# Kernel optimization log

Measured on AMD Instinct MI355X. Metric: run time of the kernel, lower is better.

The kernel has to match this reference:

```python
import jax, jax.numpy as jnp
import numpy as np

N, E, C = 100000, 50000, 256
M, D, F, T = 128, 128, 128, 64
MSG = 2 * D + F + T  # 448
T_MAX = 100000


def setup_inputs() -> dict:
    key = jax.random.key(0)
    ks = jax.random.split(key, 16)
    src = jax.random.randint(ks[0], (E,), 0, N, dtype=jnp.int32)
    dst = jax.random.randint(ks[1], (E,), 0, N, dtype=jnp.int32)
    t = jnp.sort(jax.random.randint(ks[2], (E,), 0, T_MAX, dtype=jnp.int32))
    last_update = jax.random.randint(ks[3], (N,), 0, 1000, dtype=jnp.int32)
    event_feat = jax.random.normal(ks[4], (E, F), dtype=jnp.float32)
    src_embeds = jax.random.normal(ks[5], (E, D), dtype=jnp.float32)
    dst_embeds = jax.random.normal(ks[6], (E, D), dtype=jnp.float32)
    nodes_memory = jax.random.normal(ks[7], (N, M), dtype=jnp.float32)
    incidence = jax.random.uniform(ks[8], (N, C), dtype=jnp.float32)
    w_time = jax.random.normal(ks[9], (T,), dtype=jnp.float32)
    b_time = jax.random.normal(ks[10], (T,), dtype=jnp.float32)
    W_ih = jax.random.normal(ks[11], (MSG, 3 * M), dtype=jnp.float32) * 0.05
    W_hh = jax.random.normal(ks[12], (M, 3 * M), dtype=jnp.float32) * 0.05
    b_ih = jnp.zeros((3 * M,), jnp.float32)
    b_hh = jnp.zeros((3 * M,), jnp.float32)
    return dict(src=src, dst=dst, t=t, last_update=last_update,
                event_feat=event_feat, src_embeds=src_embeds, dst_embeds=dst_embeds,
                nodes_memory=nodes_memory, incidence=incidence,
                w_time=w_time, b_time=b_time, W_ih=W_ih, W_hh=W_hh,
                b_ih=b_ih, b_hh=b_hh)


def reference(src, dst, t, last_update, event_feat, src_embeds, dst_embeds,
              nodes_memory, incidence, w_time, b_time, W_ih, W_hh, b_ih, b_hh):
    E2 = 2 * E
    # store_events: raw messages + flipped-direction messages, keyed by source node
    src_all = jnp.concatenate([src, dst])            # [2E]
    emb_s = jnp.concatenate([src_embeds, dst_embeds], axis=0)
    emb_d = jnp.concatenate([dst_embeds, src_embeds], axis=0)
    feat = jnp.concatenate([event_feat, event_feat], axis=0)
    t_all = jnp.concatenate([t, t])                  # [2E]
    # message function: concat(src_embed, dst_embed, event_feat, time_encoding(dt))
    dt = (t_all - last_update[src_all]).astype(jnp.float32)
    time_enc = jnp.cos(dt[:, None] * w_time[None, :] + b_time[None, :])  # [2E, T]
    msg = jnp.concatenate([emb_s, emb_d, feat, time_enc], axis=-1)       # [2E, MSG]
    # 'last' aggregation: per-node argmax over timestamps via rank-encoded segment_max
    perm = jnp.argsort(t_all)  # ascending time order
    rank = jnp.zeros((E2,), jnp.int32).at[perm].set(jnp.arange(E2, dtype=jnp.int32))
    seg_rank = jax.ops.segment_max(rank, src_all, num_segments=N)
    counts = jax.ops.segment_sum(jnp.ones((E2,), jnp.int32), src_all, num_segments=N)
    has_msg = counts > 0                              # [N]
    last_idx = perm[jnp.where(has_msg, seg_rank, 0)]  # [N] event index of last message
    agg_msg = msg[last_idx]                           # [N, MSG]
    # GRU memory updater (torch.nn.GRUCell convention)
    gx = agg_msg @ W_ih + b_ih
    gh = nodes_memory @ W_hh + b_hh
    xr, xz, xn = jnp.split(gx, 3, axis=-1)
    hr, hz, hn = jnp.split(gh, 3, axis=-1)
    r = jax.nn.sigmoid(xr + hr)
    z = jax.nn.sigmoid(xz + hz)
    n = jnp.tanh(xn + r * hn)
    h_new = (1.0 - z) * n + z * nodes_memory
    new_mem = jnp.where(has_msg[:, None], h_new, nodes_memory)  # [N, M]
    # rewire_graph: community memory = incidence.T @ nodes_memory
    comm_mem = jnp.einsum('nc,nm->cm', incidence, new_mem)      # [C, M]
    return jnp.concatenate([new_mem, comm_mem], axis=0)         # [N + C, M]
```

## Files before the change

### kernel.cpp

```cpp
#include <hip/hip_runtime.h>
#include <hip/hip_bf16.h>
#include <stdint.h>

#define N_NODES   100000
#define N_EVENTS  50000
#define N_COMM    256
#define DIM_M     128
#define K_TOT     576
#define GCOLS     512
#define INV2PI    0.15915494309189535f
#define XB_GRID   2048
#define WCONV_BLOCKS ((GCOLS * K_TOT + 255) / 256)
#define COPY_BLOCKS  512

typedef float f32x4 __attribute__((ext_vector_type(4)));
typedef short s16x8 __attribute__((ext_vector_type(8)));
typedef short s16x4 __attribute__((ext_vector_type(4)));

#define KEYS_OFF   0
#define CNT_OFF    800000
#define LIST_OFF   800008
#define EINFO_OFF  1200064
#define WT_OFF     2800128
#define X_ROWS     100096
#define X_OFF      3390208
#define PART_M_OFF X_OFF
#define CT_NCH     512
#define CT_CPN     196
#define TMP2_OFF   (PART_M_OFF + 67108864)
#define WT_F_OFF   1200640
#define TENC_OFF   1790464
#define PART_F_OFF 14594560

__device__ inline unsigned short f2bf(float x) {
    union { float f; unsigned u; } v; v.f = x;
    unsigned r = v.u + 0x7FFFu + ((v.u >> 16) & 1u);
    return (unsigned short)(r >> 16);
}
__device__ inline float bf2f(unsigned short u) {
    union { unsigned u; float f; } v; v.u = ((unsigned)u) << 16;
    return v.f;
}
__device__ inline float cos_rev(float rev) {
    float fr = rev - floorf(rev);
#if __has_builtin(__builtin_amdgcn_cosf)
    return __builtin_amdgcn_cosf(fr);
#else
    return cosf(fr * 6.283185307179586f);
#endif
}
__device__ inline float sigmoid_f(float x) { return 1.0f / (1.0f + __expf(-x)); }
__device__ inline float tanh_f(float x) {
    float t = __expf(2.0f * x);
    return 1.0f - 2.0f / (t + 1.0f);
}
__device__ inline s16x8 pack_bf8(float4 a, float4 b) {
    s16x8 v;
    v[0] = (short)f2bf(a.x); v[1] = (short)f2bf(a.y);
    v[2] = (short)f2bf(a.z); v[3] = (short)f2bf(a.w);
    v[4] = (short)f2bf(b.x); v[5] = (short)f2bf(b.y);
    v[6] = (short)f2bf(b.z); v[7] = (short)f2bf(b.w);
    return v;
}

__global__ __launch_bounds__(256) void k_agg(const int* __restrict__ src,
                                             const int* __restrict__ dst,
                                             const int* __restrict__ t,
                                             unsigned long long* __restrict__ keys) {
    int i = blockIdx.x * 256 + threadIdx.x;
    if (i >= 2 * N_EVENTS) return;
    int e = (i < N_EVENTS) ? i : i - N_EVENTS;
    int node = (i < N_EVENTS) ? src[i] : dst[e];
    unsigned long long key =
        ((unsigned long long)(unsigned)t[e] << 32) | (unsigned)(i + 1);
    atomicMax(&keys[node], key);
}

__global__ __launch_bounds__(256) void k_compact(const unsigned long long* __restrict__ keys,
                                                 const int* __restrict__ t,
                                                 const int* __restrict__ last_update,
                                                 unsigned int* __restrict__ cnt,
                                                 int* __restrict__ list,
                                                 int4* __restrict__ einfo) {
    int n = blockIdx.x * 256 + threadIdx.x;
    if (n >= N_NODES) return;
    const unsigned long long key = keys[n];
    if (key != 0ULL) {
        unsigned p = atomicAdd(cnt, 1u);
        list[p] = n;
        const int ia = (int)(key & 0xffffffffull) - 1;
        const int e = (ia < N_EVENTS) ? ia : ia - N_EVENTS;
        const float dt = (float)(t[e] - last_update[n]);
        einfo[p] = make_int4(n, ia, __float_as_int(dt), 0);
    }
}

__global__ __launch_bounds__(256) void k_xbuild(
    const unsigned long long* __restrict__ keys,
    const unsigned int* __restrict__ cnt,
    const int4* __restrict__ einfo,
    const float* __restrict__ event_feat,
    const float* __restrict__ src_embeds,
    const float* __restrict__ dst_embeds,
    const float* __restrict__ mem,
    const float* __restrict__ w_time,
    const float* __restrict__ b_time,
    const float* __restrict__ W_ih,
    const float* __restrict__ W_hh,
    unsigned short* __restrict__ Wt,
    unsigned short* __restrict__ X,
    float* __restrict__ out) {
    if (blockIdx.x >= XB_GRID + WCONV_BLOCKS) {
        const int b = blockIdx.x - (XB_GRID + WCONV_BLOCKS);
        for (int idx = b * 256 + threadIdx.x; idx < N_NODES * 32;
             idx += COPY_BLOCKS * 256) {
            const int n = idx >> 5;
            if (keys[n] == 0ULL)
                ((float4*)out)[idx] = ((const float4*)mem)[idx];
        }
        return;
    }
    if (blockIdx.x >= XB_GRID) {
        int idx = (blockIdx.x - XB_GRID) * 256 + threadIdx.x;
        if (idx >= GCOLS * K_TOT) return;
        int col2 = idx / K_TOT, k = idx % K_TOT;
        int mh = col2 >> 8, rem = col2 & 255;
        int g = rem >> 6, m = mh * 64 + (rem & 63);
        float v;
        if (g == 0)      v = (k < 448) ? W_ih[(size_t)k * 384 + m]
                                       : W_hh[(size_t)(k - 448) * 384 + m];
        else if (g == 1) v = (k < 448) ? W_ih[(size_t)k * 384 + 128 + m]
                                       : W_hh[(size_t)(k - 448) * 384 + 128 + m];
        else if (g == 2) v = (k < 448) ? W_ih[(size_t)k * 384 + 256 + m] : 0.0f;
        else             v = (k < 448) ? 0.0f : W_hh[(size_t)(k - 448) * 384 + 256 + m];
        Wt[idx] = f2bf(v);
        return;
    }
    const unsigned c = *cnt;
    const unsigned cpad = (c + 127u) & ~127u;
    const int l8 = threadIdx.x & 7;
    const int off = l8 * 8;
    for (unsigned row = (blockIdx.x * 256u + threadIdx.x) >> 3; row < cpad;
         row += (XB_GRID * 256u) >> 3) {
        unsigned short* xp = X + (size_t)row * K_TOT + off;
        if (row >= c) {
            s16x8 z;
#pragma unroll
            for (int q = 0; q < 8; ++q) z[q] = 0;
#pragma unroll
            for (int j = 0; j < 9; ++j) *(s16x8*)(xp + j * 64) = z;
            continue;
        }
        const int4 ei = einfo[row];
        const int ia = ei.y;
        const int e = (ia < N_EVENTS) ? ia : ia - N_EVENTS;
        const float* sp = src_embeds + (size_t)e * 128;
        const float* dp = dst_embeds + (size_t)e * 128;
        const float* pe_s = (ia < N_EVENTS) ? sp : dp;
        const float* pe_d = (ia < N_EVENTS) ? dp : sp;
        const float* pe_f = event_feat + (size_t)e * 128;
        const float* pm   = mem + (size_t)ei.x * 128;
        const float* ps[8] = {pe_s, pe_s + 64, pe_d, pe_d + 64,
                              pe_f, pe_f + 64, pm,   pm + 64};
        float4 d0[8], d1[8];
#pragma unroll
        for (int j = 0; j < 8; ++j) {
            d0[j] = *(const float4*)(ps[j] + off);
            d1[j] = *(const float4*)(ps[j] + off + 4);
        }
        const float dt = __int_as_float(ei.z);
        s16x8 tv;
#pragma unroll
        for (int q = 0; q < 8; ++q) {
            float rev = fmaf(dt, w_time[off + q] * INV2PI, b_time[off + q] * INV2PI);
            tv[q] = (short)f2bf(cos_rev(rev));
        }
#pragma unroll
        for (int j = 0; j < 6; ++j)
            *(s16x8*)(xp + j * 64) = pack_bf8(d0[j], d1[j]);
        *(s16x8*)(xp + 6 * 64) = tv;
        *(s16x8*)(xp + 7 * 64) = pack_bf8(d0[6], d1[6]);
        *(s16x8*)(xp + 8 * 64) = pack_bf8(d0[7], d1[7]);
    }
}

__global__ __launch_bounds__(512, 4) void k_gemm2(
    const unsigned int* __restrict__ cnt,
    const int* __restrict__ list,
    const unsigned short* __restrict__ X,
    const unsigned short* __restrict__ Wt,
    const float* __restrict__ b_ih,
    const float* __restrict__ b_hh,
    float* __restrict__ out) {
    __shared__ unsigned short As[3][128][32];
    __shared__ unsigned short Bs[3][256][32];
    __shared__ int Ls[128];

    const unsigned c = *cnt;
    const int rb = blockIdx.x >> 1;
    const int mh = blockIdx.x & 1;
    const int base = rb * 128;
    if ((unsigned)base >= c) return;
    const int tid = threadIdx.x;
    const int w = tid >> 6, l = tid & 63;
    const int lr = l & 15, lk = l >> 4;
    const int wm = w >> 2, wn = w & 3;

    if (tid < 128)
        Ls[tid] = ((unsigned)(base + tid) < c) ? list[base + tid] : 0;

    const int mcol = mh * 64 + wn * 16 + lr;

    unsigned short hreg[16];
#pragma unroll
    for (int rt = 0; rt < 4; ++rt)
#pragma unroll
        for (int reg = 0; reg < 4; ++reg) {
            const int r = wm * 64 + rt * 16 + lk * 4 + reg;
            hreg[rt * 4 + reg] = X[(size_t)(base + r) * K_TOT + 448 + mcol];
        }

    const int srow = tid >> 2;
    const int sd = tid & 3;
    const int ssl = (sd ^ ((srow >> 1) & 3)) << 3;
    const unsigned short* gA  = X  + (size_t)(base + srow) * K_TOT + ssl;
    const unsigned short* gB0 = Wt + (size_t)(mh * 256 + srow) * K_TOT + ssl;
    const unsigned short* gB1 = Wt + (size_t)(mh * 256 + 128 + srow) * K_TOT + ssl;

#define GLD(SRC, DST) __builtin_amdgcn_global_load_lds( \
        (const __attribute__((address_space(1))) unsigned int*)(SRC), \
        (__attribute__((address_space(3))) unsigned int*)(DST), 16, 0, 0)

    auto stage = [&](int ch, int buf) {
        GLD(gA  + ch * 32, &As[buf][w * 16][0]);
        GLD(gB0 + ch * 32, &Bs[buf][w * 16][0]);
        GLD(gB1 + ch * 32, &Bs[buf][128 + w * 16][0]);
    };

    f32x4 acc[4][4];
#pragma unroll
    for (int rt = 0; rt < 4; ++rt)
#pragma unroll
        for (int i = 0; i < 4; ++i) acc[rt][i] = (f32x4){0.f, 0.f, 0.f, 0.f};

    stage(0, 0);
    stage(1, 1);
    __syncthreads();

#pragma unroll
    for (int ch = 0; ch < 18; ++ch) {
        const int buf = ch % 3;
        if (ch <= 15) stage(ch + 2, (ch + 2) % 3);
        __builtin_amdgcn_s_setprio(1);
        s16x8 a[4];
#pragma unroll
        for (int rt = 0; rt < 4; ++rt) {
            const int r = wm * 64 + rt * 16 + lr;
            const int sl = lk ^ ((r >> 1) & 3);
            a[rt] = *(const s16x8*)&As[buf][r][sl << 3];
        }
#pragma unroll
        for (int i = 0; i < 4; ++i) {
            const int cl = i * 64 + wn * 16 + lr;
            const int slb = lk ^ ((cl >> 1) & 3);
            s16x8 b = *(const s16x8*)&Bs[buf][cl][slb << 3];
#pragma unroll
            for (int rt = 0; rt < 4; ++rt)
                acc[rt][i] = __builtin_amdgcn_mfma_f32_16x16x32_bf16(
                    a[rt], b, acc[rt][i], 0, 0, 0);
        }
        __builtin_amdgcn_s_setprio(0);
        if (ch < 17) {
            __builtin_amdgcn_sched_barrier(0);
            if (ch < 16) asm volatile("s_waitcnt vmcnt(3)" ::: "memory");
            else         asm volatile("s_waitcnt vmcnt(0)" ::: "memory");
            __builtin_amdgcn_s_barrier();
            __builtin_amdgcn_sched_barrier(0);
        }
    }

    const float b_r  = b_ih[mcol] + b_hh[mcol];
    const float b_z  = b_ih[128 + mcol] + b_hh[128 + mcol];
    const float b_xn = b_ih[256 + mcol];
    const float b_hn = b_hh[256 + mcol];
#pragma unroll
    for (int rt = 0; rt < 4; ++rt) {
#pragma unroll
        for (int reg = 0; reg < 4; ++reg) {
            const int r = wm * 64 + rt * 16 + lk * 4 + reg;
            const int grow = base + r;
            if ((unsigned)grow < c) {
                const int node = Ls[r];
                const float h = bf2f(hreg[rt * 4 + reg]);
                float rr = sigmoid_f(acc[rt][0][reg] + b_r);
                float zz = sigmoid_f(acc[rt][1][reg] + b_z);
                float nn = tanh_f(acc[rt][2][reg] + b_xn + rr * (acc[rt][3][reg] + b_hn));
                out[(size_t)node * 128 + mcol] = (1.0f - zz) * nn + zz * h;
            }
        }
    }
#undef GLD
}

__global__ __launch_bounds__(256) void k_copy(const unsigned long long* __restrict__ keys,
                                              const float* __restrict__ nm,
                                              float* __restrict__ out) {
    int idx = blockIdx.x * 256 + threadIdx.x;
    int n = idx >> 5;
    if (n >= N_NODES) return;
    if (keys[n] != 0ULL) return;
    ((float4*)out)[idx] = ((const float4*)nm)[idx];
}

__global__ __launch_bounds__(512) void k_comm_t(const float* __restrict__ inc,
                                                const float* __restrict__ nm,
                                                float* __restrict__ partials) {
    __shared__ unsigned short T[2][12288];

    const int bid = blockIdx.x;
    const int n0 = bid * CT_CPN;
    const int n1 = min(N_NODES, n0 + CT_CPN);
    const int ng = (n1 - n0 + 31) >> 5;
    const int tid = threadIdx.x;
    const int w = tid >> 6, l = tid & 63;
    const int lr = l & 15, lk = l >> 4;

    float vi[4][4];
    float vm[4][2];

    auto load_chunk = [&](int g) {
        const int nb = n0 + g * 32 + w * 4;
#pragma unroll
        for (int ri = 0; ri < 4; ++ri) {
            const int n = nb + ri;
            const bool ok = n < n1;
#pragma unroll
            for (int j = 0; j < 4; ++j)
                vi[ri][j] = ok ? inc[(size_t)n * N_COMM + l + 64 * j] : 0.0f;
#pragma unroll
            for (int j = 0; j < 2; ++j)
                vm[ri][j] = ok ? nm[(size_t)n * DIM_M + l + 64 * j] : 0.0f;
        }
    };
    auto write_chunk = [&](int buf) {
        unsigned short* bi = &T[buf][0];
#pragma unroll
        for (int j = 0; j < 4; ++j) {
            const int cc = l + 64 * j;
            ushort4 p = make_ushort4(f2bf(vi[0][j]), f2bf(vi[1][j]),
                                     f2bf(vi[2][j]), f2bf(vi[3][j]));
            *(ushort4*)&bi[cc * 32 + ((w ^ (cc & 7)) << 2)] = p;
        }
        unsigned short* bm = &T[buf][8192];
#pragma unroll
        for (int j = 0; j < 2; ++j) {
            const int mm = l + 64 * j;
            ushort4 p = make_ushort4(f2bf(vm[0][j]), f2bf(vm[1][j]),
                                     f2bf(vm[2][j]), f2bf(vm[3][j]));
            *(ushort4*)&bm[mm * 32 + ((w ^ (mm & 7)) << 2)] = p;
        }
    };

    f32x4 acc[2][8];
#pragma unroll
    for (int ct = 0; ct < 2; ++ct)
#pragma unroll
        for (int mt = 0; mt < 8; ++mt) acc[ct][mt] = (f32x4){0.f, 0.f, 0.f, 0.f};

    auto compute_chunk = [&](int buf) {
        const unsigned short* bi = &T[buf][0];
        const unsigned short* bm = &T[buf][8192];
        s16x8 a[2];
#pragma unroll
        for (int ct = 0; ct < 2; ++ct) {
            const int cc = (w * 2 + ct) * 16 + lr;
            s16x4 lo = *(const s16x4*)&bi[cc * 32 + (((lk * 2) ^ (cc & 7)) << 2)];
            s16x4 hi = *(const s16x4*)&bi[cc * 32 + (((lk * 2 + 1) ^ (cc & 7)) << 2)];
            a[ct] = __builtin_shufflevector(lo, hi, 0, 1, 2, 3, 4, 5, 6, 7);
        }
#pragma unroll
        for (int mt = 0; mt < 8; ++mt) {
            const int mm = mt * 16 + lr;
            s16x4 lo = *(const s16x4*)&bm[mm * 32 + (((lk * 2) ^ (mm & 7)) << 2)];
            s16x4 hi = *(const s16x4*)&bm[mm * 32 + (((lk * 2 + 1) ^ (mm & 7)) << 2)];
            s16x8 b = __builtin_shufflevector(lo, hi, 0, 1, 2, 3, 4, 5, 6, 7);
            acc[0][mt] = __builtin_amdgcn_mfma_f32_16x16x32_bf16(a[0], b, acc[0][mt], 0, 0, 0);
            acc[1][mt] = __builtin_amdgcn_mfma_f32_16x16x32_bf16(a[1], b, acc[1][mt], 0, 0, 0);
        }
    };

    load_chunk(0);
    write_chunk(0);
    __syncthreads();
    for (int g = 0; g < ng; ++g) {
        if (g + 1 < ng) load_chunk(g + 1);
        compute_chunk(g & 1);
        if (g + 1 < ng) write_chunk((g + 1) & 1);
        __syncthreads();
    }

    float* p = partials + (size_t)bid * (N_COMM * DIM_M);
#pragma unroll
    for (int ct = 0; ct < 2; ++ct)
#pragma unroll
        for (int mt = 0; mt < 8; ++mt)
            *(f32x4*)&p[(size_t)(((ct * 8 + mt) * 512) + tid) * 4] = acc[ct][mt];
}

__global__ __launch_bounds__(256) void k_comm2a(const float* __restrict__ partials,
                                                float* __restrict__ tmp) {
    const int bid = blockIdx.x;
    const int y = bid >> 5, x = bid & 31;
    const int idx4 = x * 256 + threadIdx.x;
    float4 s = make_float4(0.f, 0.f, 0.f, 0.f);
    for (int ci = 0; ci < CT_NCH / 32; ++ci) {
        float4 v = *(const float4*)&partials[(size_t)(y * (CT_NCH / 32) + ci) * (N_COMM * DIM_M) + idx4 * 4];
        s.x += v.x; s.y += v.y; s.z += v.z; s.w += v.w;
    }
    *(float4*)&tmp[(size_t)y * (N_COMM * DIM_M) + idx4 * 4] = s;
}

__global__ __launch_bounds__(256) void k_comm2b(const float* __restrict__ tmp,
                                                float* __restrict__ out) {
    const int idx4 = blockIdx.x * 256 + threadIdx.x;
    float4 s = make_float4(0.f, 0.f, 0.f, 0.f);
    for (int y = 0; y < 32; ++y) {
        float4 v = *(const float4*)&tmp[(size_t)y * (N_COMM * DIM_M) + idx4 * 4];
        s.x += v.x; s.y += v.y; s.z += v.z; s.w += v.w;
    }
    const int q = idx4 >> 9;
    const int tid = idx4 & 511;
    const int ct = q >> 3, mt = q & 7;
    const int w = tid >> 6, l = tid & 63;
    const int lr = l & 15, lk = l >> 4;
    const int mm = mt * 16 + lr;
    const float sv[4] = {s.x, s.y, s.z, s.w};
#pragma unroll
    for (int reg = 0; reg < 4; ++reg) {
        const int cc = (w * 2 + ct) * 16 + lk * 4 + reg;
        out[(size_t)N_NODES * DIM_M + (size_t)cc * DIM_M + mm] = sv[reg];
    }
}

__global__ __launch_bounds__(256) void k_wconv_old(const float* __restrict__ W_ih,
                                                   const float* __restrict__ W_hh,
                                                   unsigned short* __restrict__ Wt) {
    int idx = blockIdx.x * 256 + threadIdx.x;
    if (idx >= GCOLS * K_TOT) return;
    int col = idx / K_TOT, k = idx % K_TOT;
    float v;
    if (col < 256) {
        v = (k < 448) ? W_ih[(size_t)k * 384 + col]
                      : W_hh[(size_t)(k - 448) * 384 + col];
    } else if (col < 384) {
        v = (k < 448) ? W_ih[(size_t)k * 384 + col] : 0.0f;
    } else {
        v = (k < 448) ? 0.0f : W_hh[(size_t)(k - 448) * 384 + (col - 128)];
    }
    Wt[idx] = f2bf(v);
}

__global__ __launch_bounds__(256) void k_tenc(const unsigned long long* __restrict__ keys,
                                              const unsigned int* __restrict__ cnt,
                                              const int* __restrict__ list,
                                              const int* __restrict__ t,
                                              const int* __restrict__ last_update,
                                              const float* __restrict__ w_time,
                                              const float* __restrict__ b_time,
                                              unsigned short* __restrict__ tenc) {
    int idx = blockIdx.x * 256 + threadIdx.x;
    int r = idx >> 3, slot = idx & 7;
    const unsigned c = *cnt;
    const unsigned cpad = (c + 63u) & ~63u;
    if ((unsigned)r >= cpad) return;
    s16x8 v;
    if ((unsigned)r < c) {
        int node = list[r];
        unsigned long long key = keys[node];
        int ia = (int)(key & 0xffffffffull) - 1;
        int e = (ia < N_EVENTS) ? ia : ia - N_EVENTS;
        float dt = (float)(t[e] - last_update[node]);
#pragma unroll
        for (int j = 0; j < 8; ++j) {
            int cix = slot * 8 + j;
            float arg = __fadd_rn(__fmul_rn(dt, w_time[cix]), b_time[cix]);
            v[j] = (short)f2bf(cosf(arg));
        }
    } else {
#pragma unroll
        for (int j = 0; j < 8; ++j) v[j] = 0;
    }
    *(s16x8*)&tenc[(size_t)r * 64 + slot * 8] = v;
}

__global__ __launch_bounds__(256, 2) void k_gemm_fused(
    const unsigned long long* __restrict__ keys,
    const unsigned int* __restrict__ cnt,
    const int* __restrict__ list,
    const float* __restrict__ event_feat,
    const float* __restrict__ src_embeds,
    const float* __restrict__ dst_embeds,
    const float* __restrict__ mem,
    const unsigned short* __restrict__ tenc,
    const unsigned short* __restrict__ Wt,
    const float* __restrict__ b_ih,
    const float* __restrict__ b_hh,
    float* __restrict__ out) {
    __shared__ unsigned short Xs[2][4][64][8];

    const unsigned c = *cnt;
    const int base = blockIdx.x * 64;
    if ((unsigned)base >= c) return;
    const int tid = threadIdx.x;

    const int srow = tid >> 2;
    const int kslot = tid & 3;
    const int sgrow = base + srow;
    const bool valid = (unsigned)sgrow < c;
    const float *p_es = nullptr, *p_ed = nullptr, *p_ef = nullptr, *p_mem = nullptr;
    const unsigned short* p_te = nullptr;
    if (valid) {
        int node = list[sgrow];
        unsigned long long key = keys[node];
        int ia = (int)(key & 0xffffffffull) - 1;
        int e = (ia < N_EVENTS) ? ia : ia - N_EVENTS;
        const float* sp = src_embeds + (size_t)e * 128;
        const float* dp = dst_embeds + (size_t)e * 128;
        p_es = (ia < N_EVENTS) ? sp : dp;
        p_ed = (ia < N_EVENTS) ? dp : sp;
        p_ef = event_feat + (size_t)e * 128;
        p_te = tenc + (size_t)sgrow * 64;
        p_mem = mem + (size_t)node * 128;
    }

    auto stage = [&](int ch) {
        const int buf = ch & 1;
        const int k0 = ch * 32 + kslot * 8;
        s16x8 v;
        if (valid) {
            if (k0 < 384) {
                const float* p = (k0 < 128) ? (p_es + k0)
                               : (k0 < 256) ? (p_ed + (k0 - 128))
                                            : (p_ef + (k0 - 256));
                float4 a = *(const float4*)p;
                float4 b = *(const float4*)(p + 4);
                v = pack_bf8(a, b);
            } else if (k0 < 448) {
                v = *(const s16x8*)(p_te + (k0 - 384));
            } else {
                const float* p = p_mem + (k0 - 448);
                float4 a = *(const float4*)p;
                float4 b = *(const float4*)(p + 4);
                v = pack_bf8(a, b);
            }
        } else {
#pragma unroll
            for (int j = 0; j < 8; ++j) v[j] = 0;
        }
        *(s16x8*)&Xs[buf][kslot][srow][0] = v;
    };

    const int w = tid >> 6;
    const int l = tid & 63;
    const int lr = l & 15;
    const int lk = l >> 4;

    f32x4 acc[4][8];
#pragma unroll
    for (int rt = 0; rt < 4; ++rt)
#pragma unroll
        for (int i = 0; i < 8; ++i) acc[rt][i] = (f32x4){0.f, 0.f, 0.f, 0.f};

    stage(0);
    __syncthreads();

    for (int ch = 0; ch < 18; ++ch) {
        if (ch < 17) stage(ch + 1);
        const int buf = ch & 1;
        s16x8 a[4];
#pragma unroll
        for (int rt = 0; rt < 4; ++rt)
            a[rt] = *(const s16x8*)&Xs[buf][lk][rt * 16 + lr][0];
#pragma unroll
        for (int i = 0; i < 8; ++i) {
            const int col = (w + 4 * i) * 16 + lr;
            s16x8 b = *(const s16x8*)&Wt[(size_t)col * K_TOT + ch * 32 + lk * 8];
#pragma unroll
            for (int rt = 0; rt < 4; ++rt)
                acc[rt][i] = __builtin_amdgcn_mfma_f32_16x16x32_bf16(
                    a[rt], b, acc[rt][i], 0, 0, 0);
        }
        __syncthreads();
    }

#pragma unroll
    for (int jj = 0; jj < 2; ++jj) {
        const int mcol = (w + 4 * jj) * 16 + lr;
        const float b_r  = b_ih[mcol] + b_hh[mcol];
        const float b_z  = b_ih[128 + mcol] + b_hh[128 + mcol];
        const float b_xn = b_ih[256 + mcol];
        const float b_hn = b_hh[256 + mcol];
#pragma unroll
        for (int rt = 0; rt < 4; ++rt) {
#pragma unroll
            for (int reg = 0; reg < 4; ++reg) {
                const int grow = base + rt * 16 + lk * 4 + reg;
                if ((unsigned)grow < c) {
                    const int node = list[grow];
                    const float h = mem[(size_t)node * 128 + mcol];
                    float rr = sigmoid_f(acc[rt][0 + jj][reg] + b_r);
                    float zz = sigmoid_f(acc[rt][2 + jj][reg] + b_z);
                    float nn = tanh_f(acc[rt][4 + jj][reg] + b_xn +
                                      rr * (acc[rt][6 + jj][reg] + b_hn));
                    out[(size_t)node * 128 + mcol] = (1.0f - zz) * nn + zz * h;
                }
            }
        }
    }
}

__global__ __launch_bounds__(256) void k_comm1(const float* __restrict__ inc,
                                               const float* __restrict__ nm,
                                               float* __restrict__ partials,
                                               int nch, int cpn) {
    __shared__ float inc_s[2][8][128];
    __shared__ float mem_s[2][8][128];

    const int bid = blockIdx.x;
    const int ct2 = bid / nch;
    const int ch  = bid % nch;
    const int n0 = ch * cpn;
    const int n1 = min(N_NODES, n0 + cpn);
    const int tid = threadIdx.x;

    const int srow = tid >> 5;
    const int scol = (tid & 31) * 4;

    auto stage = [&](int g, int buf) {
        const int n = n0 + g * 8 + srow;
        float4 iv = make_float4(0.f, 0.f, 0.f, 0.f);
        float4 mv = make_float4(0.f, 0.f, 0.f, 0.f);
        if (n < n1) {
            iv = *(const float4*)(inc + (size_t)n * N_COMM + ct2 * 128 + scol);
            mv = *(const float4*)(nm + (size_t)n * DIM_M + scol);
        }
        *(float4*)&inc_s[buf][srow][scol] = iv;
        *(float4*)&mem_s[buf][srow][scol] = mv;
    };

    const int c0 = (tid >> 3) * 4;
    const int mb = (tid & 7) * 4;

    float acc[4][4][4];
#pragma unroll
    for (int a = 0; a < 4; ++a)
#pragma unroll
        for (int b = 0; b < 4; ++b)
#pragma unroll
            for (int d = 0; d < 4; ++d) acc[a][b][d] = 0.0f;

    const int ngrp = (n1 - n0 + 7) >> 3;
    stage(0, 0);
    __syncthreads();

    for (int g = 0; g < ngrp; ++g) {
        if (g + 1 < ngrp) stage(g + 1, (g + 1) & 1);
        const int buf = g & 1;
#pragma unroll
        for (int i = 0; i < 8; ++i) {
            const float4 cv = *(const float4*)&inc_s[buf][i][c0];
            const float ca[4] = {cv.x, cv.y, cv.z, cv.w};
#pragma unroll
            for (int j = 0; j < 4; ++j) {
                const float4 mv = *(const float4*)&mem_s[buf][i][j * 32 + mb];
                const float ma[4] = {mv.x, mv.y, mv.z, mv.w};
#pragma unroll
                for (int ci = 0; ci < 4; ++ci)
#pragma unroll
                    for (int mi = 0; mi < 4; ++mi)
                        acc[ci][j][mi] = fmaf(ca[ci], ma[mi], acc[ci][j][mi]);
            }
        }
        __syncthreads();
    }

    float* p = partials + (size_t)bid * (128 * 128);
#pragma unroll
    for (int ci = 0; ci < 4; ++ci)
#pragma unroll
        for (int j = 0; j < 4; ++j)
            *(float4*)(p + (size_t)(c0 + ci) * 128 + j * 32 + mb) =
                make_float4(acc[ci][j][0], acc[ci][j][1], acc[ci][j][2], acc[ci][j][3]);
}

__global__ __launch_bounds__(256) void k_comm2_f(const float* __restrict__ partials,
                                                 float* __restrict__ out,
                                                 int nch) {
    int idx = blockIdx.x * 256 + threadIdx.x;
    if (idx >= N_COMM * DIM_M) return;
    int cg = idx >> 7;
    int m = idx & 127;
    int ct2 = cg >> 7;
    int cl = cg & 127;
    float s = 0.0f;
    for (int ch = 0; ch < nch; ++ch)
        s += partials[((size_t)ct2 * nch + ch) * 16384 + (size_t)cl * 128 + m];
    out[(size_t)N_NODES * DIM_M + idx] = s;
}

extern "C" void kernel_launch(void* const* d_in, const int* in_sizes, int n_in,
                              void* d_out, int out_size, void* d_ws, size_t ws_size,
                              hipStream_t stream) {
    const int* src          = (const int*)d_in[0];
    const int* dst          = (const int*)d_in[1];
    const int* t            = (const int*)d_in[2];
    const int* last_update  = (const int*)d_in[3];
    const float* event_feat = (const float*)d_in[4];
    const float* src_embeds = (const float*)d_in[5];
    const float* dst_embeds = (const float*)d_in[6];
    const float* nodes_mem  = (const float*)d_in[7];
    const float* incidence  = (const float*)d_in[8];
    const float* w_time     = (const float*)d_in[9];
    const float* b_time     = (const float*)d_in[10];
    const float* W_ih       = (const float*)d_in[11];
    const float* W_hh       = (const float*)d_in[12];
    const float* b_ih       = (const float*)d_in[13];
    const float* b_hh       = (const float*)d_in[14];
    float* out = (float*)d_out;

    char* ws = (char*)d_ws;
    unsigned long long* keys = (unsigned long long*)(ws + KEYS_OFF);
    unsigned int* cnt        = (unsigned int*)(ws + CNT_OFF);
    int* list                = (int*)(ws + LIST_OFF);
    int4* einfo              = (int4*)(ws + EINFO_OFF);

    const bool xfit = ws_size >= (size_t)X_OFF + (size_t)X_ROWS * (K_TOT * 2);

    hipMemsetAsync(d_ws, 0, LIST_OFF, stream);

    k_agg<<<(2 * N_EVENTS + 255) / 256, 256, 0, stream>>>(src, dst, t, keys);
    k_compact<<<(N_NODES + 255) / 256, 256, 0, stream>>>(keys, t, last_update,
                                                         cnt, list, einfo);

    if (xfit) {
        unsigned short* Wt = (unsigned short*)(ws + WT_OFF);
        unsigned short* X  = (unsigned short*)(ws + X_OFF);
        float* partials    = (float*)(ws + PART_M_OFF);
        float* tmp2        = (float*)(ws + TMP2_OFF);

        k_xbuild<<<XB_GRID + WCONV_BLOCKS + COPY_BLOCKS, 256, 0, stream>>>(
            keys, cnt, einfo, event_feat, src_embeds, dst_embeds,
            nodes_mem, w_time, b_time, W_ih, W_hh, Wt, X, out);
        k_gemm2<<<(X_ROWS / 128) * 2, 512, 0, stream>>>(cnt, list, X, Wt,
                                                        b_ih, b_hh, out);
        k_comm_t<<<CT_NCH, 512, 0, stream>>>(incidence, out, partials);
        k_comm2a<<<1024, 256, 0, stream>>>(partials, tmp2);
        k_comm2b<<<32, 256, 0, stream>>>(tmp2, out);
    } else {
        unsigned short* Wt   = (unsigned short*)(ws + WT_F_OFF);
        unsigned short* tenc = (unsigned short*)(ws + TENC_OFF);
        float* partials      = (float*)(ws + PART_F_OFF);
        int NCH = 512;
        while (NCH > 8 && (size_t)PART_F_OFF + (size_t)NCH * 131072 > ws_size) NCH >>= 1;
        int cpn = (N_NODES + NCH - 1) / NCH;

        k_wconv_old<<<(GCOLS * K_TOT + 255) / 256, 256, 0, stream>>>(W_ih, W_hh, Wt);
        k_tenc<<<(100032 * 8) / 256, 256, 0, stream>>>(keys, cnt, list, t, last_update,
                                                       w_time, b_time, tenc);
        k_gemm_fused<<<100032 / 64, 256, 0, stream>>>(keys, cnt, list, event_feat,
                                                      src_embeds, dst_embeds, nodes_mem,
                                                      tenc, Wt, b_ih, b_hh, out);
        k_copy<<<(N_NODES * 32 + 255) / 256, 256, 0, stream>>>(keys, nodes_mem, out);
        k_comm1<<<2 * NCH, 256, 0, stream>>>(incidence, out, partials, NCH, cpn);
        k_comm2_f<<<(N_COMM * DIM_M + 255) / 256, 256, 0, stream>>>(partials, out, NCH);
    }
}
```

Baseline: 210.4 us.

## Replace node-scan compaction with event-based flag/scan/emit compaction

Removes the single global atomic counter that handed out list slots as nodes were scanned. Instead, each event checks whether it won the atomicMax for its node, blocks count their winners, a single-block scan computes offsets, and a second pass writes list and einfo at those offsets. This trades one kernel for three small launches and reads src/dst/keys twice, in exchange for avoiding contention on the global atomic. The resulting list order is event order rather than node order, which may change the memory access pattern in later gather stages.

```diff
diff --git a/kernel.cpp b/kernel.cpp
--- a/kernel.cpp
+++ b/kernel.cpp
@@ -12,6 +12,7 @@
 #define XB_GRID   2048
 #define WCONV_BLOCKS ((GCOLS * K_TOT + 255) / 256)
 #define COPY_BLOCKS  512
+#define NBLK      ((2 * N_EVENTS + 255) / 256)
 
 typedef float f32x4 __attribute__((ext_vector_type(4)));
 typedef short s16x8 __attribute__((ext_vector_type(8)));
@@ -28,9 +29,13 @@
 #define CT_NCH     512
 #define CT_CPN     196
 #define TMP2_OFF   (PART_M_OFF + 67108864)
+#define BCNT_OFF   TMP2_OFF
+#define BOFF_OFF   (TMP2_OFF + 2048)
 #define WT_F_OFF   1200640
 #define TENC_OFF   1790464
 #define PART_F_OFF 14594560
+#define BCNT_F_OFF PART_F_OFF
+#define BOFF_F_OFF (PART_F_OFF + 2048)
 
 __device__ inline unsigned short f2bf(float x) {
     union { float f; unsigned u; } v; v.f = x;
@@ -76,22 +81,66 @@
     atomicMax(&keys[node], key);
 }
 
-__global__ __launch_bounds__(256) void k_compact(const unsigned long long* __restrict__ keys,
-                                                 const int* __restrict__ t,
-                                                 const int* __restrict__ last_update,
-                                                 unsigned int* __restrict__ cnt,
-                                                 int* __restrict__ list,
-                                                 int4* __restrict__ einfo) {
-    int n = blockIdx.x * 256 + threadIdx.x;
-    if (n >= N_NODES) return;
-    const unsigned long long key = keys[n];
-    if (key != 0ULL) {
-        unsigned p = atomicAdd(cnt, 1u);
-        list[p] = n;
-        const int ia = (int)(key & 0xffffffffull) - 1;
-        const int e = (ia < N_EVENTS) ? ia : ia - N_EVENTS;
-        const float dt = (float)(t[e] - last_update[n]);
-        einfo[p] = make_int4(n, ia, __float_as_int(dt), 0);
+__global__ __launch_bounds__(256) void k_flag(const int* __restrict__ src,
+                                              const int* __restrict__ dst,
+                                              const unsigned long long* __restrict__ keys,
+                                              unsigned* __restrict__ bcount) {
+    const int i = blockIdx.x * 256 + threadIdx.x;
+    int win = 0;
+    if (i < 2 * N_EVENTS) {
+        int e = (i < N_EVENTS) ? i : i - N_EVENTS;
+        int node = (i < N_EVENTS) ? src[i] : dst[e];
+        win = ((unsigned)(keys[node] & 0xffffffffull) == (unsigned)(i + 1));
+    }
+    __shared__ unsigned cnt_s;
+    if (threadIdx.x == 0) cnt_s = 0;
+    __syncthreads();
+    unsigned long long m = __ballot(win);
+    if ((threadIdx.x & 63) == 0) atomicAdd(&cnt_s, (unsigned)__popcll(m));
+    __syncthreads();
+    if (threadIdx.x == 0) bcount[blockIdx.x] = cnt_s;
+}
+
+__global__ __launch_bounds__(512) void k_scan(const unsigned* __restrict__ bcount,
+                                              unsigned* __restrict__ boff,
+                                              unsigned int* __restrict__ cnt) {
+    __shared__ unsigned s[512];
+    const int tid = threadIdx.x;
+    unsigned v = (tid < NBLK) ? bcount[tid] : 0;
+    s[tid] = v;
+    __syncthreads();
+    for (int off = 1; off < 512; off <<= 1) {
+        unsigned tv = (tid >= off) ? s[tid - off] : 0;
+        __syncthreads();
+        s[tid] += tv;
+        __syncthreads();
+    }
+    if (tid < NBLK) boff[tid] = s[tid] - v;
+    if (tid == NBLK - 1) *cnt = s[tid];
+}
+
+__global__ __launch_bounds__(256) void k_emit(const int* __restrict__ src,
+                                              const int* __restrict__ dst,
+                                              const int* __restrict__ t,
+                                              const int* __restrict__ last_update,
+                                              const unsigned long long* __restrict__ keys,
+                                              const unsigned* __restrict__ boff,
+                                              int* __restrict__ list,
+                                              int4* __restrict__ einfo) {
+    const int i = blockIdx.x * 256 + threadIdx.x;
+    __shared__ unsigned lcnt;
+    if (threadIdx.x == 0) lcnt = 0;
+    __syncthreads();
+    if (i < 2 * N_EVENTS) {
+        const int e = (i < N_EVENTS) ? i : i - N_EVENTS;
+        const int node = (i < N_EVENTS) ? src[i] : dst[e];
+        if ((unsigned)(keys[node] & 0xffffffffull) == (unsigned)(i + 1)) {
+            unsigned r = atomicAdd(&lcnt, 1u);
+            unsigned pos = boff[blockIdx.x] + r;
+            list[pos] = node;
+            const float dt = (float)(t[e] - last_update[node]);
+            einfo[pos] = make_int4(node, i, __float_as_int(dt), 0);
+        }
     }
 }
 
@@ -736,11 +785,16 @@
 
     const bool xfit = ws_size >= (size_t)X_OFF + (size_t)X_ROWS * (K_TOT * 2);
 
+    unsigned* bcount = (unsigned*)(ws + (xfit ? BCNT_OFF : BCNT_F_OFF));
+    unsigned* boff   = (unsigned*)(ws + (xfit ? BOFF_OFF : BOFF_F_OFF));
+
     hipMemsetAsync(d_ws, 0, LIST_OFF, stream);
 
     k_agg<<<(2 * N_EVENTS + 255) / 256, 256, 0, stream>>>(src, dst, t, keys);
-    k_compact<<<(N_NODES + 255) / 256, 256, 0, stream>>>(keys, t, last_update,
-                                                         cnt, list, einfo);
+    k_flag<<<NBLK, 256, 0, stream>>>(src, dst, keys, bcount);
+    k_scan<<<1, 512, 0, stream>>>(bcount, boff, cnt);
+    k_emit<<<NBLK, 256, 0, stream>>>(src, dst, t, last_update, keys, boff,
+                                     list, einfo);
 
     if (xfit) {
         unsigned short* Wt = (unsigned short*)(ws + WT_OFF);
```

New measurement: 199.0 us, median of 3. 1.06x faster.
